# Kernel optimization log

Hardware: AMD Instinct MI355X
Metric: run time of the kernel (lower is better)

## Reference

```python
import jax, jax.numpy as jnp
import numpy as np

D_K = 64
SCALE = 1.0 / (D_K ** 0.5)
NEG = -1.0e9

def setup_inputs() -> dict:
    key = jax.random.key(0)
    kq, kk, kv, km = jax.random.split(key, 4)
    B, H, S, D = 4, 16, 2048, D_K
    query = jax.random.normal(kq, (B, H, S, D), dtype=jnp.float32)
    k_ = jax.random.normal(kk, (B, H, S, D), dtype=jnp.float32)
    v_ = jax.random.normal(kv, (B, H, S, D), dtype=jnp.float32)
    mask = jax.random.randint(km, (B, 1, S, S), 0, 2, dtype=jnp.int32)
    return {"query": query, "key": k_, "value": v_, "mask": mask}

def reference(query, key, value, mask):
    # scores: [B, H, S, S]
    scores = jnp.einsum('bhqd,bhkd->bhqk', query, key) * SCALE
    scores = jnp.where(mask == 0, NEG, scores)
    attn = jax.nn.softmax(scores, axis=-1)
    return jnp.einsum('bhqk,bhkd->bhqd', attn, value)
```

## Files before the change

### kernel.cpp

```cpp
#include <hip/hip_runtime.h>

typedef _Float16 f16x8 __attribute__((ext_vector_type(8)));
typedef _Float16 f16x4 __attribute__((ext_vector_type(4)));
typedef _Float16 f16x2 __attribute__((ext_vector_type(2)));
typedef float    f32x4 __attribute__((ext_vector_type(4)));
typedef unsigned u32x4 __attribute__((ext_vector_type(4)));
typedef unsigned long long u64;

constexpr int Bc = 4, Hc = 16, Sc = 2048, Dc = 64;
constexpr int KVBLK = 64;
constexpr int NKV = Sc / KVBLK;
constexpr int QB  = 128;
constexpr int NQT = Sc / QB;
constexpr int NQ  = 32;

__device__ __forceinline__ float fast_exp2(float x) {
#if __has_builtin(__builtin_amdgcn_exp2f)
  return __builtin_amdgcn_exp2f(x);
#else
  return exp2f(x);
#endif
}

__device__ __forceinline__ void gload16(const void* g, void* l) {
  __builtin_amdgcn_global_load_lds(
      (const __attribute__((address_space(1))) void*)g,
      (__attribute__((address_space(3))) void*)l, 16, 0, 0);
}

__device__ __forceinline__ f32x4 mfma16(f16x8 a, f16x8 b, f32x4 c) {
  return __builtin_amdgcn_mfma_f32_16x16x32_f16(a, b, c, 0, 0, 0);
}

__device__ __forceinline__ float dot2acc(unsigned pk, float acc) {
#if __has_builtin(__builtin_amdgcn_fdot2)
  const f16x2 one2 = {(_Float16)1.f, (_Float16)1.f};
  return __builtin_amdgcn_fdot2(__builtin_bit_cast(f16x2, pk), one2, acc, false);
#else
  const f16x2 v = __builtin_bit_cast(f16x2, pk);
  return acc + (float)v[0] + (float)v[1];
#endif
}

__global__ __launch_bounds__(256)
void cvt_k_sw(const float* __restrict__ K, _Float16* __restrict__ Ko) {
  const int tile = blockIdx.x;
  const int t = threadIdx.x;
  const float* src = K + (size_t)tile * 4096;
  _Float16* dst = Ko + (size_t)tile * 4096;
  #pragma unroll
  for (int cc = 0; cc < 2; ++cc) {
    const int c = t + cc * 256;
    const int r = c >> 3, s = c & 7;
    const int ss = s ^ (r & 7);
    const float* p = src + r * 64 + ss * 8;
    const float4 a = *(const float4*)p;
    const float4 b2 = *(const float4*)(p + 4);
    f16x8 h = {(_Float16)a.x, (_Float16)a.y, (_Float16)a.z, (_Float16)a.w,
               (_Float16)b2.x, (_Float16)b2.y, (_Float16)b2.z, (_Float16)b2.w};
    *(f16x8*)(dst + (size_t)c * 8) = h;
  }
}

__global__ __launch_bounds__(256)
void cvt_v_sw(const float* __restrict__ V, _Float16* __restrict__ Vo) {
  __shared__ float tile[64][65];
  const int tb = blockIdx.x;
  const int t = threadIdx.x;
  const float* src = V + (size_t)tb * 4096;
  {
    const int r = t >> 2, c0 = (t & 3) * 16;
    #pragma unroll
    for (int j = 0; j < 16; j += 4)
      *(float4*)&tile[r][c0 + j] = *(const float4*)(src + r * 64 + c0 + j);
  }
  __syncthreads();
  _Float16* dst = Vo + (size_t)tb * 4096;
  #pragma unroll
  for (int cc = 0; cc < 2; ++cc) {
    const int c = t + cc * 256;
    const int d = c >> 3, ss = c & 7;
    const int m = ss ^ (d & 7);
    const int ks = m >> 2, lg = m & 3;
    f16x8 h;
    #pragma unroll
    for (int e = 0; e < 8; ++e) {
      const int key = 32 * ks + 16 * (e >> 2) + 4 * lg + (e & 3);
      h[e] = (_Float16)tile[key][d];
    }
    *(f16x8*)(dst + (size_t)c * 8) = h;
  }
}

__global__ __launch_bounds__(256)
void pack_mask(const int* __restrict__ M, u64* __restrict__ MB) {
  const int gid  = blockIdx.x * 256 + threadIdx.x;
  const int wv   = gid >> 6, lane = gid & 63;
  const int kv   = wv & (NKV - 1);
  const int row  = (wv >> 5) & (Sc - 1);
  const int b    = wv >> 16;
  const int m    = M[((size_t)b * Sc + row) * Sc + (size_t)kv * 64 + lane];
  const u64 bits = __ballot(m != 0);
  if (lane == 0)
    MB[(((size_t)b * NQ + (row >> 6)) * NKV + kv) * 64 + (row & 63)] = bits;
}

__global__ __launch_bounds__(512, 8)
void attn_fwd7(const float* __restrict__ Q, const _Float16* __restrict__ Ksw,
               const _Float16* __restrict__ Vsw, const u64* __restrict__ MB,
               float* __restrict__ O)
{
  const int bid = (blockIdx.x & 7) * 128 + (blockIdx.x >> 3);
  const int qt  = bid & (NQT - 1);
  const int bh  = bid >> 4;
  const int b   = bh >> 4;
  const int q0  = qt * QB;

  const int tid = threadIdx.x;
  const int w   = tid >> 6;
  const int l   = tid & 63;
  const int lg  = l >> 4;
  const int lc  = l & 15;

  __shared__ _Float16 SB[16384];
  const char* sb = (const char*)SB;

  const int a0 = lc * 128 + (((0 + lg) ^ (lc & 7)) << 4);
  const int a1 = lc * 128 + (((4 + lg) ^ (lc & 7)) << 4);

  f16x8 qf[2];
  {
    const float qs = 0.125f * 1.4426950408889634f;
    const float* qr = Q + ((size_t)bh * Sc + q0 + w * 16 + lc) * Dc + 8 * lg;
    #pragma unroll
    for (int ks = 0; ks < 2; ++ks) {
      f16x8 t;
      #pragma unroll
      for (int e = 0; e < 8; ++e) t[e] = (_Float16)(qr[ks * 32 + e] * qs);
      qf[ks] = t;
    }
  }

  f32x4 o_acc[4];
  #pragma unroll
  for (int nt = 0; nt < 4; ++nt) o_acc[nt] = (f32x4){0.f, 0.f, 0.f, 0.f};
  float l_acc = 0.f;
  const float NEGL = -1.4426950e9f;

  const char* KswT = (const char*)(Ksw + (size_t)bh * Sc * Dc);
  const char* VswT = (const char*)(Vsw + (size_t)bh * Sc * Dc);
  const int row = q0 + w * 16 + lc;
  const u64* Mb = MB + ((size_t)(b * NQ + (row >> 6)) * NKV) * 64 + (row & 63);

  auto stage = [&](int kvt, int buf) {
    const char* g = (w < 4) ? KswT + (size_t)kvt * 8192 + w * 2048
                            : VswT + (size_t)kvt * 8192 + (w - 4) * 2048;
    char* lb = (char*)SB + buf * 16384 + ((w < 4) ? w * 2048 : 8192 + (w - 4) * 2048);
    gload16(g + l * 16, lb);
    gload16(g + 1024 + l * 16, lb + 1024);
  };

  auto body = [&](int buf, u64 mbits) {
    const int base = buf * 16384;
    const unsigned mlo = (unsigned)mbits;
    const unsigned mhi = (unsigned)(mbits >> 32);
    u32x4 w0, w1;
    #pragma unroll
    for (int nt = 0; nt < 4; ++nt) {
      const f16x8 k0 = *(const f16x8*)(sb + base + nt * 2048 + a0);
      const f16x8 k1 = *(const f16x8*)(sb + base + nt * 2048 + a1);
      __builtin_amdgcn_s_setprio(1);
      f32x4 acc = (f32x4){0.f, 0.f, 0.f, 0.f};
      acc = mfma16(k0, qf[0], acc);
      acc = mfma16(k1, qf[1], acc);
      __builtin_amdgcn_s_setprio(0);
      const unsigned b4 = (((nt < 2) ? mlo : mhi) >> ((nt & 1) * 16 + 4 * lg)) & 0xFu;
      #pragma unroll
      for (int r = 0; r < 4; ++r)
        acc[r] = fast_exp2(((b4 >> r) & 1u) ? acc[r] : NEGL);
      const unsigned px = __builtin_bit_cast(unsigned, __builtin_amdgcn_cvt_pkrtz(acc[0], acc[1]));
      const unsigned py = __builtin_bit_cast(unsigned, __builtin_amdgcn_cvt_pkrtz(acc[2], acc[3]));
      l_acc = dot2acc(px, l_acc);
      l_acc = dot2acc(py, l_acc);
      if (nt == 0)      { w0[0] = px; w0[1] = py; }
      else if (nt == 1) { w0[2] = px; w0[3] = py; }
      else if (nt == 2) { w1[0] = px; w1[1] = py; }
      else              { w1[2] = px; w1[3] = py; }
    }
    const f16x8 pa0 = __builtin_bit_cast(f16x8, w0);
    const f16x8 pa1 = __builtin_bit_cast(f16x8, w1);

    __builtin_amdgcn_s_setprio(1);
    #pragma unroll
    for (int nt = 0; nt < 4; ++nt) {
      const f16x8 v0 = *(const f16x8*)(sb + base + 8192 + nt * 2048 + a0);
      const f16x8 v1 = *(const f16x8*)(sb + base + 8192 + nt * 2048 + a1);
      o_acc[nt] = mfma16(pa0, v0, o_acc[nt]);
      o_acc[nt] = mfma16(pa1, v1, o_acc[nt]);
    }
    __builtin_amdgcn_s_setprio(0);
  };

  u64 mb_next = Mb[0];
  stage(0, 0);
  __syncthreads();
  for (int kv = 0; kv < NKV; kv += 2) {
    const u64 mb0 = mb_next;
    const u64 mb1 = Mb[(size_t)(kv + 1) * 64];
    stage(kv + 1, 1);
    body(0, mb0);
    __syncthreads();
    if (kv + 2 < NKV) {
      mb_next = Mb[(size_t)(kv + 2) * 64];
      stage(kv + 2, 0);
    }
    body(1, mb1);
    __syncthreads();
  }

  l_acc += __shfl_xor(l_acc, 16, 64);
  l_acc += __shfl_xor(l_acc, 32, 64);
  #pragma unroll
  for (int r = 0; r < 4; ++r) {
    const float li = 1.0f / __shfl(l_acc, 4 * lg + r, 64);
    float* orow = O + ((size_t)bh * Sc + q0 + w * 16 + 4 * lg + r) * Dc + lc;
    #pragma unroll
    for (int nt = 0; nt < 4; ++nt)
      orow[nt * 16] = o_acc[nt][r] * li;
  }
}

constexpr int LDSW = KVBLK + 8;

__global__ __launch_bounds__(256)
void attn_fwd_v1(const float* __restrict__ Q, const float* __restrict__ K,
                 const float* __restrict__ V, const int* __restrict__ M,
                 float* __restrict__ O)
{
  const int bid   = blockIdx.x;
  const int qtile = bid & 31;
  const int bh    = bid >> 5;
  const int b     = bh >> 4;

  const float* Qp = Q + ((size_t)bh * Sc + (size_t)qtile * 64) * Dc;
  const float* Kp = K + (size_t)bh * Sc * Dc;
  const float* Vp = V + (size_t)bh * Sc * Dc;
  const int*   Mp = M + (size_t)b * Sc * Sc + (size_t)qtile * 64 * Sc;
  float*       Op = O + ((size_t)bh * Sc + (size_t)qtile * 64) * Dc;

  __shared__ _Float16 Klds [KVBLK][LDSW];
  __shared__ _Float16 Vtlds[Dc]   [LDSW];
  __shared__ _Float16 Pl   [64]   [LDSW];

  const int tid = threadIdx.x;
  const int w   = tid >> 6;
  const int l   = tid & 63;
  const int lg  = l >> 4;
  const int lc  = l & 15;

  f16x8 qf[2];
  {
    const float qs = 0.125f * 1.4426950408889634f;
    const float* qrow = Qp + (size_t)(w * 16 + lc) * Dc + 8 * lg;
    #pragma unroll
    for (int ks = 0; ks < 2; ++ks) {
      f16x8 t;
      #pragma unroll
      for (int e = 0; e < 8; ++e) t[e] = (_Float16)(qrow[ks * 32 + e] * qs);
      qf[ks] = t;
    }
  }

  f32x4 o_acc[4];
  #pragma unroll
  for (int nt = 0; nt < 4; ++nt) o_acc[nt] = (f32x4){0.f, 0.f, 0.f, 0.f};
  float m_r[4], l_r[4];
  #pragma unroll
  for (int r = 0; r < 4; ++r) { m_r[r] = -3.0e38f; l_r[r] = 0.f; }
  const float NEGL = -1.4426950e9f;

  for (int kv = 0; kv < NKV; ++kv) {
    const float* Kt = Kp + (size_t)kv * KVBLK * Dc;
    const float* Vt = Vp + (size_t)kv * KVBLK * Dc;
    __syncthreads();
    {
      const int r = tid >> 2, c0 = (tid & 3) * 16;
      const float* src = Kt + (size_t)r * Dc + c0;
      f16x8 h0, h1;
      #pragma unroll
      for (int e = 0; e < 8; ++e) h0[e] = (_Float16)src[e];
      #pragma unroll
      for (int e = 0; e < 8; ++e) h1[e] = (_Float16)src[8 + e];
      *(f16x8*)&Klds[r][c0]     = h0;
      *(f16x8*)&Klds[r][c0 + 8] = h1;
    }
    {
      const int r0 = (tid >> 4) * 4, c0 = (tid & 15) * 4;
      float a_[4][4];
      #pragma unroll
      for (int i = 0; i < 4; ++i) {
        const float4 v4 = *(const float4*)(Vt + (size_t)(r0 + i) * Dc + c0);
        a_[i][0] = v4.x; a_[i][1] = v4.y; a_[i][2] = v4.z; a_[i][3] = v4.w;
      }
      #pragma unroll
      for (int j = 0; j < 4; ++j) {
        f16x4 t = {(_Float16)a_[0][j], (_Float16)a_[1][j],
                   (_Float16)a_[2][j], (_Float16)a_[3][j]};
        *(f16x4*)&Vtlds[c0 + j][r0] = t;
      }
    }
    __syncthreads();

    f32x4 s_acc[4];
    #pragma unroll
    for (int nt = 0; nt < 4; ++nt) {
      f32x4 acc = (f32x4){0.f, 0.f, 0.f, 0.f};
      #pragma unroll
      for (int ks = 0; ks < 2; ++ks) {
        f16x8 kf = *(const f16x8*)&Klds[nt * 16 + lc][ks * 32 + 8 * lg];
        acc = __builtin_amdgcn_mfma_f32_16x16x32_f16(qf[ks], kf, acc, 0, 0, 0);
      }
      s_acc[nt] = acc;
    }

    const int* mbase = Mp + (size_t)kv * KVBLK + lc;
    #pragma unroll
    for (int r = 0; r < 4; ++r) {
      const int qrow = w * 16 + 4 * lg + r;
      const int* mr = mbase + (size_t)qrow * Sc;
      float s0 = (mr[0]  != 0) ? s_acc[0][r] : NEGL;
      float s1 = (mr[16] != 0) ? s_acc[1][r] : NEGL;
      float s2 = (mr[32] != 0) ? s_acc[2][r] : NEGL;
      float s3 = (mr[48] != 0) ? s_acc[3][r] : NEGL;
      float mx = fmaxf(fmaxf(s0, s1), fmaxf(s2, s3));
      #pragma unroll
      for (int off = 1; off < 16; off <<= 1)
        mx = fmaxf(mx, __shfl_xor(mx, off, 64));
      const float mn   = fmaxf(m_r[r], mx);
      const float corr = fast_exp2(m_r[r] - mn);
      m_r[r] = mn;
      float p0 = fast_exp2(s0 - mn);
      float p1 = fast_exp2(s1 - mn);
      float p2 = fast_exp2(s2 - mn);
      float p3 = fast_exp2(s3 - mn);
      float rs = (p0 + p1) + (p2 + p3);
      #pragma unroll
      for (int off = 1; off < 16; off <<= 1)
        rs += __shfl_xor(rs, off, 64);
      l_r[r] = l_r[r] * corr + rs;
      #pragma unroll
      for (int nt = 0; nt < 4; ++nt) o_acc[nt][r] *= corr;
      Pl[qrow][lc]      = (_Float16)p0;
      Pl[qrow][16 + lc] = (_Float16)p1;
      Pl[qrow][32 + lc] = (_Float16)p2;
      Pl[qrow][48 + lc] = (_Float16)p3;
    }

    #pragma unroll
    for (int nt = 0; nt < 4; ++nt) {
      #pragma unroll
      for (int ks = 0; ks < 2; ++ks) {
        f16x8 pf = *(const f16x8*)&Pl[w * 16 + lc][ks * 32 + 8 * lg];
        f16x8 vf = *(const f16x8*)&Vtlds[nt * 16 + lc][ks * 32 + 8 * lg];
        o_acc[nt] = __builtin_amdgcn_mfma_f32_16x16x32_f16(pf, vf, o_acc[nt], 0, 0, 0);
      }
    }
  }

  #pragma unroll
  for (int r = 0; r < 4; ++r) {
    const float inv = 1.0f / l_r[r];
    float* orow = Op + (size_t)(w * 16 + 4 * lg + r) * Dc;
    #pragma unroll
    for (int nt = 0; nt < 4; ++nt)
      orow[nt * 16 + lc] = o_acc[nt][r] * inv;
  }
}

extern "C" void kernel_launch(void* const* d_in, const int* in_sizes, int n_in,
                              void* d_out, int out_size, void* d_ws, size_t ws_size,
                              hipStream_t stream) {
  (void)in_sizes; (void)n_in; (void)out_size;
  const float* Q = (const float*)d_in[0];
  const float* K = (const float*)d_in[1];
  const float* V = (const float*)d_in[2];
  const int*   M = (const int*)d_in[3];
  float*       O = (float*)d_out;

  const size_t nKV      = (size_t)Bc * Hc * Sc * Dc;
  const size_t bytesK16 = nKV * 2;
  const size_t bytesMB  = (size_t)Bc * NQ * NKV * 64 * 8;
  const size_t need     = 2 * bytesK16 + bytesMB;

  if (ws_size >= need) {
    _Float16* K16  = (_Float16*)d_ws;
    _Float16* Vt16 = (_Float16*)((char*)d_ws + bytesK16);
    u64*      MBp  = (u64*)((char*)d_ws + 2 * bytesK16);
    hipLaunchKernelGGL(cvt_k_sw,  dim3(2048),  dim3(256), 0, stream, K, K16);
    hipLaunchKernelGGL(cvt_v_sw,  dim3(2048),  dim3(256), 0, stream, V, Vt16);
    hipLaunchKernelGGL(pack_mask, dim3(65536), dim3(256), 0, stream, M, MBp);
    hipLaunchKernelGGL(attn_fwd7, dim3(1024),  dim3(512), 0, stream, Q, K16, Vt16, MBp, O);
  } else {
    hipLaunchKernelGGL(attn_fwd_v1, dim3(2048), dim3(256), 0, stream, Q, K, V, M, O);
  }
}
```

Measured before the change: 136.2 us.

## Switch attention MFMA to 32x32x16 tiles with 4-wave blocks

Rewrites the main attention kernel to use 32x32x16 f16 MFMA instead of 16x16x32. Each wave now owns 32 query rows, and blocks shrink from 8 to 4 waves while still covering 128 queries. The V pre-swizzle kernel changes its key permutation to match the new operand layout, and staging issues four loads per wave. Larger MFMA tiles reuse each LDS fragment more and cut the number of instructions, at the cost of more accumulator registers per lane and lower occupancy.

```diff
diff --git a/kernel.cpp b/kernel.cpp
--- a/kernel.cpp
+++ b/kernel.cpp
@@ -4,6 +4,7 @@
 typedef _Float16 f16x4 __attribute__((ext_vector_type(4)));
 typedef _Float16 f16x2 __attribute__((ext_vector_type(2)));
 typedef float    f32x4 __attribute__((ext_vector_type(4)));
+typedef float    f32x16 __attribute__((ext_vector_type(16)));
 typedef unsigned u32x4 __attribute__((ext_vector_type(4)));
 typedef unsigned long long u64;
 
@@ -28,8 +29,12 @@
       (__attribute__((address_space(3))) void*)l, 16, 0, 0);
 }
 
-__device__ __forceinline__ f32x4 mfma16(f16x8 a, f16x8 b, f32x4 c) {
-  return __builtin_amdgcn_mfma_f32_16x16x32_f16(a, b, c, 0, 0, 0);
+__device__ __forceinline__ f32x16 mfma32(f16x8 a, f16x8 b, f32x16 c) {
+  return __builtin_amdgcn_mfma_f32_32x32x16_f16(a, b, c, 0, 0, 0);
+}
+
+__device__ __forceinline__ unsigned pkrtz(float x, float y) {
+  return __builtin_bit_cast(unsigned, __builtin_amdgcn_cvt_pkrtz(x, y));
 }
 
 __device__ __forceinline__ float dot2acc(unsigned pk, float acc) {
@@ -40,6 +45,13 @@
   const f16x2 v = __builtin_bit_cast(f16x2, pk);
   return acc + (float)v[0] + (float)v[1];
 #endif
+}
+
+__device__ __forceinline__ f32x16 zero16() {
+  f32x16 z;
+  #pragma unroll
+  for (int i = 0; i < 16; ++i) z[i] = 0.f;
+  return z;
 }
 
 __global__ __launch_bounds__(256)
@@ -63,7 +75,7 @@
 }
 
 __global__ __launch_bounds__(256)
-void cvt_v_sw(const float* __restrict__ V, _Float16* __restrict__ Vo) {
+void cvt_v_sw2(const float* __restrict__ V, _Float16* __restrict__ Vo) {
   __shared__ float tile[64][65];
   const int tb = blockIdx.x;
   const int t = threadIdx.x;
@@ -79,13 +91,13 @@
   #pragma unroll
   for (int cc = 0; cc < 2; ++cc) {
     const int c = t + cc * 256;
-    const int d = c >> 3, ss = c & 7;
-    const int m = ss ^ (d & 7);
-    const int ks = m >> 2, lg = m & 3;
+    const int d = c >> 3, cpos = c & 7;
+    const int cl = cpos ^ (d & 7);
     f16x8 h;
     #pragma unroll
     for (int e = 0; e < 8; ++e) {
-      const int key = 32 * ks + 16 * (e >> 2) + 4 * lg + (e & 3);
+      const int kap = cl * 8 + e;
+      const int key = (kap & 51) | ((kap & 4) << 1) | ((kap & 8) >> 1);
       h[e] = (_Float16)tile[key][d];
     }
     *(f16x8*)(dst + (size_t)c * 8) = h;
@@ -105,8 +117,8 @@
     MB[(((size_t)b * NQ + (row >> 6)) * NKV + kv) * 64 + (row & 63)] = bits;
 }
 
-__global__ __launch_bounds__(512, 8)
-void attn_fwd7(const float* __restrict__ Q, const _Float16* __restrict__ Ksw,
+__global__ __launch_bounds__(256, 4)
+void attn_fwd8(const float* __restrict__ Q, const _Float16* __restrict__ Ksw,
                const _Float16* __restrict__ Vsw, const u64* __restrict__ MB,
                float* __restrict__ O)
 {
@@ -119,85 +131,121 @@
   const int tid = threadIdx.x;
   const int w   = tid >> 6;
   const int l   = tid & 63;
-  const int lg  = l >> 4;
-  const int lc  = l & 15;
+  const int q5  = l & 31;
+  const int hb  = l >> 5;
+  const int xb  = q5 & 7;
 
   __shared__ _Float16 SB[16384];
   const char* sb = (const char*)SB;
 
-  const int a0 = lc * 128 + (((0 + lg) ^ (lc & 7)) << 4);
-  const int a1 = lc * 128 + (((4 + lg) ^ (lc & 7)) << 4);
-
-  f16x8 qf[2];
+  int as_[4];
+  #pragma unroll
+  for (int s = 0; s < 4; ++s)
+    as_[s] = q5 * 128 + (((((s << 1) | hb)) ^ xb) << 4);
+
+  f16x8 qf[4];
   {
     const float qs = 0.125f * 1.4426950408889634f;
-    const float* qr = Q + ((size_t)bh * Sc + q0 + w * 16 + lc) * Dc + 8 * lg;
-    #pragma unroll
-    for (int ks = 0; ks < 2; ++ks) {
-      f16x8 t;
-      #pragma unroll
-      for (int e = 0; e < 8; ++e) t[e] = (_Float16)(qr[ks * 32 + e] * qs);
-      qf[ks] = t;
-    }
-  }
-
-  f32x4 o_acc[4];
-  #pragma unroll
-  for (int nt = 0; nt < 4; ++nt) o_acc[nt] = (f32x4){0.f, 0.f, 0.f, 0.f};
+    const float* qr = Q + ((size_t)bh * Sc + q0 + w * 32 + q5) * Dc + 8 * hb;
+    #pragma unroll
+    for (int s = 0; s < 4; ++s) {
+      const float4 f0 = *(const float4*)(qr + s * 16);
+      const float4 f1 = *(const float4*)(qr + s * 16 + 4);
+      f16x8 t = {(_Float16)(f0.x * qs), (_Float16)(f0.y * qs),
+                 (_Float16)(f0.z * qs), (_Float16)(f0.w * qs),
+                 (_Float16)(f1.x * qs), (_Float16)(f1.y * qs),
+                 (_Float16)(f1.z * qs), (_Float16)(f1.w * qs)};
+      qf[s] = t;
+    }
+  }
+
+  f32x16 o0 = zero16(), o1 = zero16();
   float l_acc = 0.f;
   const float NEGL = -1.4426950e9f;
 
   const char* KswT = (const char*)(Ksw + (size_t)bh * Sc * Dc);
   const char* VswT = (const char*)(Vsw + (size_t)bh * Sc * Dc);
-  const int row = q0 + w * 16 + lc;
+  const int row = q0 + w * 32 + q5;
   const u64* Mb = MB + ((size_t)(b * NQ + (row >> 6)) * NKV) * 64 + (row & 63);
 
   auto stage = [&](int kvt, int buf) {
-    const char* g = (w < 4) ? KswT + (size_t)kvt * 8192 + w * 2048
-                            : VswT + (size_t)kvt * 8192 + (w - 4) * 2048;
-    char* lb = (char*)SB + buf * 16384 + ((w < 4) ? w * 2048 : 8192 + (w - 4) * 2048);
-    gload16(g + l * 16, lb);
-    gload16(g + 1024 + l * 16, lb + 1024);
+    const char* g = (w < 2) ? KswT + (size_t)kvt * 8192 + (w & 1) * 4096
+                            : VswT + (size_t)kvt * 8192 + (w & 1) * 4096;
+    char* lb = (char*)SB + buf * 16384 + ((w < 2) ? 0 : 8192) + (w & 1) * 4096;
+    #pragma unroll
+    for (int j = 0; j < 4; ++j)
+      gload16(g + j * 1024 + l * 16, lb + j * 1024);
   };
 
   auto body = [&](int buf, u64 mbits) {
     const int base = buf * 16384;
-    const unsigned mlo = (unsigned)mbits;
-    const unsigned mhi = (unsigned)(mbits >> 32);
-    u32x4 w0, w1;
-    #pragma unroll
-    for (int nt = 0; nt < 4; ++nt) {
-      const f16x8 k0 = *(const f16x8*)(sb + base + nt * 2048 + a0);
-      const f16x8 k1 = *(const f16x8*)(sb + base + nt * 2048 + a1);
-      __builtin_amdgcn_s_setprio(1);
-      f32x4 acc = (f32x4){0.f, 0.f, 0.f, 0.f};
-      acc = mfma16(k0, qf[0], acc);
-      acc = mfma16(k1, qf[1], acc);
-      __builtin_amdgcn_s_setprio(0);
-      const unsigned b4 = (((nt < 2) ? mlo : mhi) >> ((nt & 1) * 16 + 4 * lg)) & 0xFu;
-      #pragma unroll
-      for (int r = 0; r < 4; ++r)
-        acc[r] = fast_exp2(((b4 >> r) & 1u) ? acc[r] : NEGL);
-      const unsigned px = __builtin_bit_cast(unsigned, __builtin_amdgcn_cvt_pkrtz(acc[0], acc[1]));
-      const unsigned py = __builtin_bit_cast(unsigned, __builtin_amdgcn_cvt_pkrtz(acc[2], acc[3]));
-      l_acc = dot2acc(px, l_acc);
-      l_acc = dot2acc(py, l_acc);
-      if (nt == 0)      { w0[0] = px; w0[1] = py; }
-      else if (nt == 1) { w0[2] = px; w0[3] = py; }
-      else if (nt == 2) { w1[0] = px; w1[1] = py; }
-      else              { w1[2] = px; w1[3] = py; }
-    }
-    const f16x8 pa0 = __builtin_bit_cast(f16x8, w0);
-    const f16x8 pa1 = __builtin_bit_cast(f16x8, w1);
-
+    f32x16 acc0 = zero16(), acc1 = zero16();
     __builtin_amdgcn_s_setprio(1);
     #pragma unroll
-    for (int nt = 0; nt < 4; ++nt) {
-      const f16x8 v0 = *(const f16x8*)(sb + base + 8192 + nt * 2048 + a0);
-      const f16x8 v1 = *(const f16x8*)(sb + base + 8192 + nt * 2048 + a1);
-      o_acc[nt] = mfma16(pa0, v0, o_acc[nt]);
-      o_acc[nt] = mfma16(pa1, v1, o_acc[nt]);
-    }
+    for (int s = 0; s < 4; ++s) {
+      const f16x8 k0 = *(const f16x8*)(sb + base + as_[s]);
+      acc0 = mfma32(k0, qf[s], acc0);
+    }
+    #pragma unroll
+    for (int s = 0; s < 4; ++s) {
+      const f16x8 k1 = *(const f16x8*)(sb + base + 4096 + as_[s]);
+      acc1 = mfma32(k1, qf[s], acc1);
+    }
+    __builtin_amdgcn_s_setprio(0);
+
+    u32x4 pw0, pw1, pw2, pw3;
+    {
+      const unsigned mh = (unsigned)mbits;
+      #pragma unroll
+      for (int b2 = 0; b2 < 4; ++b2) {
+        const unsigned nib = (mh >> (8 * b2 + 4 * hb)) & 0xFu;
+        #pragma unroll
+        for (int a2 = 0; a2 < 4; ++a2) {
+          const int r = 4 * b2 + a2;
+          acc0[r] = fast_exp2(((nib >> a2) & 1u) ? acc0[r] : NEGL);
+        }
+      }
+      #pragma unroll
+      for (int i = 0; i < 4; ++i) {
+        pw0[i] = pkrtz(acc0[2 * i], acc0[2 * i + 1]);
+        pw1[i] = pkrtz(acc0[8 + 2 * i], acc0[8 + 2 * i + 1]);
+        l_acc = dot2acc(pw0[i], l_acc);
+        l_acc = dot2acc(pw1[i], l_acc);
+      }
+    }
+    {
+      const unsigned mh = (unsigned)(mbits >> 32);
+      #pragma unroll
+      for (int b2 = 0; b2 < 4; ++b2) {
+        const unsigned nib = (mh >> (8 * b2 + 4 * hb)) & 0xFu;
+        #pragma unroll
+        for (int a2 = 0; a2 < 4; ++a2) {
+          const int r = 4 * b2 + a2;
+          acc1[r] = fast_exp2(((nib >> a2) & 1u) ? acc1[r] : NEGL);
+        }
+      }
+      #pragma unroll
+      for (int i = 0; i < 4; ++i) {
+        pw2[i] = pkrtz(acc1[2 * i], acc1[2 * i + 1]);
+        pw3[i] = pkrtz(acc1[8 + 2 * i], acc1[8 + 2 * i + 1]);
+        l_acc = dot2acc(pw2[i], l_acc);
+        l_acc = dot2acc(pw3[i], l_acc);
+      }
+    }
+    const f16x8 pa0 = __builtin_bit_cast(f16x8, pw0);
+    const f16x8 pa1 = __builtin_bit_cast(f16x8, pw1);
+    const f16x8 pa2 = __builtin_bit_cast(f16x8, pw2);
+    const f16x8 pa3 = __builtin_bit_cast(f16x8, pw3);
+
+    __builtin_amdgcn_s_setprio(1);
+    o0 = mfma32(pa0, *(const f16x8*)(sb + base + 8192 + as_[0]), o0);
+    o0 = mfma32(pa1, *(const f16x8*)(sb + base + 8192 + as_[1]), o0);
+    o0 = mfma32(pa2, *(const f16x8*)(sb + base + 8192 + as_[2]), o0);
+    o0 = mfma32(pa3, *(const f16x8*)(sb + base + 8192 + as_[3]), o0);
+    o1 = mfma32(pa0, *(const f16x8*)(sb + base + 12288 + as_[0]), o1);
+    o1 = mfma32(pa1, *(const f16x8*)(sb + base + 12288 + as_[1]), o1);
+    o1 = mfma32(pa2, *(const f16x8*)(sb + base + 12288 + as_[2]), o1);
+    o1 = mfma32(pa3, *(const f16x8*)(sb + base + 12288 + as_[3]), o1);
     __builtin_amdgcn_s_setprio(0);
   };
 
@@ -218,15 +266,14 @@
     __syncthreads();
   }
 
-  l_acc += __shfl_xor(l_acc, 16, 64);
   l_acc += __shfl_xor(l_acc, 32, 64);
   #pragma unroll
-  for (int r = 0; r < 4; ++r) {
-    const float li = 1.0f / __shfl(l_acc, 4 * lg + r, 64);
-    float* orow = O + ((size_t)bh * Sc + q0 + w * 16 + 4 * lg + r) * Dc + lc;
-    #pragma unroll
-    for (int nt = 0; nt < 4; ++nt)
-      orow[nt * 16] = o_acc[nt][r] * li;
+  for (int reg = 0; reg < 16; ++reg) {
+    const int qrow = (reg & 3) + 8 * (reg >> 2) + 4 * hb;
+    const float li = 1.0f / __shfl(l_acc, qrow, 64);
+    float* op = O + ((size_t)bh * Sc + q0 + w * 32 + qrow) * Dc + q5;
+    op[0]  = o0[reg] * li;
+    op[32] = o1[reg] * li;
   }
 }
 
@@ -396,10 +443,10 @@
     _Float16* K16  = (_Float16*)d_ws;
     _Float16* Vt16 = (_Float16*)((char*)d_ws + bytesK16);
     u64*      MBp  = (u64*)((char*)d_ws + 2 * bytesK16);
-    hipLaunchKernelGGL(cvt_k_sw,  dim3(2048),  dim3(256), 0, stream, K, K16);
-    hipLaunchKernelGGL(cvt_v_sw,  dim3(2048),  dim3(256), 0, stream, V, Vt16);
-    hipLaunchKernelGGL(pack_mask, dim3(65536), dim3(256), 0, stream, M, MBp);
-    hipLaunchKernelGGL(attn_fwd7, dim3(1024),  dim3(512), 0, stream, Q, K16, Vt16, MBp, O);
+    hipLaunchKernelGGL(cvt_k_sw,   dim3(2048),  dim3(256), 0, stream, K, K16);
+    hipLaunchKernelGGL(cvt_v_sw2,  dim3(2048),  dim3(256), 0, stream, V, Vt16);
+    hipLaunchKernelGGL(pack_mask,  dim3(65536), dim3(256), 0, stream, M, MBp);
+    hipLaunchKernelGGL(attn_fwd8,  dim3(1024),  dim3(256), 0, stream, Q, K16, Vt16, MBp, O);
   } else {
     hipLaunchKernelGGL(attn_fwd_v1, dim3(2048), dim3(256), 0, stream, Q, K, V, M, O);
   }
```

After: 136.4 us. No clear change (+0.2%).
